# Performance work log

Measured on AMD Instinct MI355X. Metric: run time of the kernel, lower is better.

The kernel has to match this reference:

```python
import jax, jax.numpy as jnp
import numpy as np

D = 1024; HEADS = 16; DH = D // HEADS; DEPTH = 8; FACT = 2
EPS = 1e-6


def _rmsnorm(x):
    return x * jax.lax.rsqrt(jnp.mean(x * x, axis=-1, keepdims=True) + EPS)


def _rope(x, pos):
    # x: [N, H, T, d]; pos: [T]. Standard rotate-half RoPE on dim d.
    d = x.shape[-1]
    half = d // 2
    inv_freq = 1.0 / (10000.0 ** (jnp.arange(half, dtype=x.dtype) / half))
    ang = pos[:, None] * inv_freq  # [T, half]
    cos = jnp.concatenate([jnp.cos(ang), jnp.cos(ang)], axis=-1)  # [T, d]
    sin = jnp.concatenate([jnp.sin(ang), jnp.sin(ang)], axis=-1)
    rot = jnp.concatenate([-x[..., half:], x[..., :half]], axis=-1)
    return x * cos + rot * sin


def _apply_rope_2d(q, k, pos_h, pos_w):
    # Split head_dim in half: first half rotated by row position, second by column.
    dh = q.shape[-1] // 2
    q = jnp.concatenate([_rope(q[..., :dh], pos_h), _rope(q[..., dh:], pos_w)], axis=-1)
    k = jnp.concatenate([_rope(k[..., :dh], pos_h), _rope(k[..., dh:], pos_w)], axis=-1)
    return q, k


def setup_inputs() -> dict:
    key = jax.random.key(0)
    ks = jax.random.split(key, 8)
    s = 0.02
    f32 = jnp.float32
    return {
        "x": jax.random.normal(ks[0], (4, 16, 64, 64), f32),
        "merge_w": (jax.random.normal(ks[1], (D, 16 * FACT * FACT), f32) * s),
        "qkv_w": (jax.random.normal(ks[2], (DEPTH, 3 * D, D), f32) * s),
        "qkv_b": jnp.zeros((DEPTH, 3 * D), f32),
        "proj_w": (jax.random.normal(ks[3], (DEPTH, D, D), f32) * s),
        "proj_b": jnp.zeros((DEPTH, D), f32),
        "fc1_w": (jax.random.normal(ks[4], (DEPTH, 4 * D, D), f32) * s),
        "fc1_b": jnp.zeros((DEPTH, 4 * D), f32),
        "fc2_w": (jax.random.normal(ks[5], (DEPTH, D, 4 * D), f32) * s),
        "fc2_b": jnp.zeros((DEPTH, D), f32),
    }


def reference(x, merge_w, qkv_w, qkv_b, proj_w, proj_b, fc1_w, fc1_b, fc2_w, fc2_b):
    N, C, H, W = x.shape
    Hf, Wf = H // FACT, W // FACT
    L = Hf * Wf
    # SpatialMerger: unfold(k=f,s=f) channel order is (c, kh, kw)
    patches = x.reshape(N, C, Hf, FACT, Wf, FACT)
    patches = patches.transpose(0, 2, 4, 1, 3, 5).reshape(N, L, C * FACT * FACT)
    tok = patches @ merge_w.T  # [N, L, D], bias=False

    pos_h = jnp.repeat(jnp.arange(Hf, dtype=tok.dtype), Wf)  # [L]
    pos_w = jnp.tile(jnp.arange(Wf, dtype=tok.dtype), Hf)
    scale = 1.0 / np.sqrt(DH)

    for i in range(DEPTH):
        h = _rmsnorm(tok)
        qkv = h @ qkv_w[i].T + qkv_b[i]  # [N, L, 3D]
        q, k, v = jnp.split(qkv, 3, axis=-1)
        q = q.reshape(N, L, HEADS, DH).transpose(0, 2, 1, 3)  # [N, Hh, T, Dh]
        k = k.reshape(N, L, HEADS, DH).transpose(0, 2, 1, 3)
        v = v.reshape(N, L, HEADS, DH).transpose(0, 2, 1, 3)
        q, k = _apply_rope_2d(q, k, pos_h, pos_w)
        attn = jnp.einsum('nhtd,nhsd->nhts', q, k) * scale
        p = jax.nn.softmax(attn, axis=-1)
        o = jnp.einsum('nhts,nhsd->nhtd', p, v)
        o = o.transpose(0, 2, 1, 3).reshape(N, L, D)
        tok = tok + (o @ proj_w[i].T + proj_b[i])

        h = _rmsnorm(tok)
        hidden = jax.nn.gelu(h @ fc1_w[i].T + fc1_b[i], approximate=True)
        tok = tok + (hidden @ fc2_w[i].T + fc2_b[i])

    z_seq = _rmsnorm(tok)          # [N, L, D]
    z = z_seq.transpose(0, 2, 1)   # [N, D, L]
    return z
```

## Files before the change

kernel.cpp:

```cpp
#include <hip/hip_runtime.h>
#include <hip/hip_bf16.h>
#include <cmath>

typedef __bf16 bf16_t;
typedef __bf16 bf16x4 __attribute__((ext_vector_type(4)));
typedef __bf16 bf16x8 __attribute__((ext_vector_type(8)));
typedef float f32x4 __attribute__((ext_vector_type(4)));

typedef const __attribute__((address_space(1))) void gv_t;
typedef __attribute__((address_space(3))) void sv_t;

#define GLDS16(g, l) __builtin_amdgcn_global_load_lds((gv_t*)(g), (sv_t*)(l), 16, 0, 0)

template <int EPI>
__global__ __launch_bounds__(256, 2) void gemm128(
    const bf16_t* __restrict__ A, const bf16_t* __restrict__ B,
    const float* __restrict__ bias, float* __restrict__ Cf,
    bf16_t* __restrict__ Cb, int N, int K, int KS)
{
    __shared__ __align__(16) bf16_t As[3][128 * 32];
    __shared__ __align__(16) bf16_t Bs[3][128 * 32];
    const int tid = threadIdx.x;
    const int bm = blockIdx.x, bn = blockIdx.y, bz = blockIdx.z;
    const int wave = tid >> 6, lane = tid & 63;
    const int wr = (wave >> 1) << 6, wc = (wave & 1) << 6;
    const int lr = lane & 15, kq = (lane >> 4) << 3;

    f32x4 acc[4][4] = {};

    const int kbeg = bz * KS;
    const bf16_t* gA = A + (size_t)(bm * 128 + (tid >> 2)) * K + (tid & 3) * 8 + kbeg;
    const bf16_t* gB = B + (size_t)(bn * 128 + (tid >> 2)) * K + (tid & 3) * 8 + kbeg;
    const bf16_t* gA2 = gA + (size_t)64 * K;
    const bf16_t* gB2 = gB + (size_t)64 * K;
    const int dst = tid * 8;
    const int nt = KS >> 5;

#define STAGE(buf, t) do { const int _k = (t) << 5;          \
        GLDS16(gA  + _k, As[buf] + dst);                     \
        GLDS16(gA2 + _k, As[buf] + dst + 2048);              \
        GLDS16(gB  + _k, Bs[buf] + dst);                     \
        GLDS16(gB2 + _k, Bs[buf] + dst + 2048); } while (0)

    STAGE(0, 0);
    if (nt > 1) STAGE(1, 1);
    int cur = 0, pre = 2;
    for (int t = 0; t < nt; ++t) {
        if (t + 1 < nt) asm volatile("s_waitcnt vmcnt(4)" ::: "memory");
        else            asm volatile("s_waitcnt vmcnt(0)" ::: "memory");
        __builtin_amdgcn_s_barrier();
        if (t + 2 < nt) STAGE(pre, t + 2);

        const bf16_t* Ac = As[cur];
        const bf16_t* Bc = Bs[cur];
        bf16x8 af[4], bfr[4];
#pragma unroll
        for (int i = 0; i < 4; i++)
            af[i] = *(const bf16x8*)(Ac + (wr + i * 16 + lr) * 32 + kq);
#pragma unroll
        for (int j = 0; j < 4; j++)
            bfr[j] = *(const bf16x8*)(Bc + (wc + j * 16 + lr) * 32 + kq);
#pragma unroll
        for (int i = 0; i < 4; i++)
#pragma unroll
            for (int j = 0; j < 4; j++)
                acc[i][j] = __builtin_amdgcn_mfma_f32_16x16x32_bf16(af[i], bfr[j], acc[i][j], 0, 0, 0);

        cur = (cur == 2) ? 0 : cur + 1;
        pre = (pre == 2) ? 0 : pre + 1;
    }
#undef STAGE

    const int row0 = bm * 128 + wr + ((lane >> 4) << 2);
    const int col0 = bn * 128 + wc + lr;

    if constexpr (EPI == 6) {
        float bv[4];
#pragma unroll
        for (int j = 0; j < 4; j++) bv[j] = bias[col0 + j * 16];
        const bool doRope = (col0 < 2048);
        const float invf = exp2f(-0.83048202372184056f * (float)lr);
#pragma unroll
        for (int i = 0; i < 4; i++) {
#pragma unroll
            for (int r = 0; r < 4; r++) {
                const int row = row0 + i * 16 + r;
                float v0 = acc[i][0][r] + bv[0], v1 = acc[i][1][r] + bv[1];
                float v2 = acc[i][2][r] + bv[2], v3 = acc[i][3][r] + bv[3];
                if (doRope) {
                    const int tt = row & 1023;
                    float s0, c0, s1, c1;
                    sincosf((float)(tt >> 5) * invf, &s0, &c0);
                    sincosf((float)(tt & 31) * invf, &s1, &c1);
                    float o0 = v0 * c0 - v1 * s0, o1 = v1 * c0 + v0 * s0;
                    float o2 = v2 * c1 - v3 * s1, o3 = v3 * c1 + v2 * s1;
                    v0 = o0; v1 = o1; v2 = o2; v3 = o3;
                }
                bf16_t* cp = Cb + (size_t)row * N + col0;
                cp[0] = (bf16_t)v0; cp[16] = (bf16_t)v1;
                cp[32] = (bf16_t)v2; cp[48] = (bf16_t)v3;
            }
        }
        return;
    }

#pragma unroll
    for (int j = 0; j < 4; j++) {
        const int col = col0 + j * 16;
        float bv = 0.f;
        if constexpr (EPI == 5) { if (bz == 0) bv = bias[col]; }
        else if constexpr (EPI != 0) bv = bias[col];
#pragma unroll
        for (int i = 0; i < 4; i++) {
#pragma unroll
            for (int r = 0; r < 4; r++) {
                const int row = row0 + i * 16 + r;
                float v = acc[i][j][r] + bv;
                if constexpr (EPI == 0) {
                    Cf[(size_t)row * N + col] = v;
                } else if constexpr (EPI == 5) {
                    atomicAdd(&Cf[(size_t)row * 1024 + col], v);
                } else if constexpr (EPI == 3) {
                    float g = 0.5f * v * (1.f + tanhf(0.7978845608f * (v + 0.044715f * v * v * v)));
                    Cb[(size_t)row * N + col] = (bf16_t)g;
                } else {
                    Cb[(size_t)row * N + col] = (bf16_t)v;
                }
            }
        }
    }
}

__global__ __launch_bounds__(256) void convw_k(
    const float* __restrict__ q, const float* __restrict__ p,
    const float* __restrict__ f1, const float* __restrict__ f2,
    bf16_t* __restrict__ oq, bf16_t* __restrict__ op,
    bf16_t* __restrict__ of1, bf16_t* __restrict__ of2)
{
    int idx = blockIdx.x * 256 + threadIdx.x;
    const float* src; bf16_t* dst; int off;
    if (idx < 786432)       { src = q;  dst = oq;  off = idx; }
    else if (idx < 1048576) { src = p;  dst = op;  off = idx - 786432; }
    else if (idx < 2097152) { src = f1; dst = of1; off = idx - 1048576; }
    else                    { src = f2; dst = of2; off = idx - 2097152; }
    float4 v = ((const float4*)src)[off];
    bf16x4 o; o[0] = (bf16_t)v.x; o[1] = (bf16_t)v.y; o[2] = (bf16_t)v.z; o[3] = (bf16_t)v.w;
    *(bf16x4*)(dst + (size_t)off * 4) = o;
}

__global__ __launch_bounds__(256) void cvt_k(const float* __restrict__ in, bf16_t* __restrict__ out)
{
    int idx = blockIdx.x * 256 + threadIdx.x;
    float4 v = ((const float4*)in)[idx];
    bf16x4 o; o[0] = (bf16_t)v.x; o[1] = (bf16_t)v.y; o[2] = (bf16_t)v.z; o[3] = (bf16_t)v.w;
    *(bf16x4*)(out + (size_t)idx * 4) = o;
}

__global__ __launch_bounds__(256) void patches_k(const float* __restrict__ x, bf16_t* __restrict__ out)
{
    int idx = blockIdx.x * 256 + threadIdx.x;
    int cc = idx & 63, l = (idx >> 6) & 1023, n = idx >> 16;
    int c = cc >> 2, kh = (cc >> 1) & 1, kw = cc & 1;
    int hf = l >> 5, wf = l & 31;
    out[idx] = (bf16_t)x[(((n * 16 + c) * 64) + hf * 2 + kh) * 64 + wf * 2 + kw];
}

__global__ __launch_bounds__(256) void rmsnorm_k(const float* __restrict__ tok, bf16_t* __restrict__ out)
{
    int row = blockIdx.x, tid = threadIdx.x;
    float4 xv = ((const float4*)(tok + (size_t)row * 1024))[tid];
    float s = xv.x * xv.x + xv.y * xv.y + xv.z * xv.z + xv.w * xv.w;
#pragma unroll
    for (int off = 32; off > 0; off >>= 1) s += __shfl_down(s, off, 64);
    __shared__ float ws4[4];
    if ((tid & 63) == 0) ws4[tid >> 6] = s;
    __syncthreads();
    float sc = rsqrtf((ws4[0] + ws4[1] + ws4[2] + ws4[3]) * (1.f / 1024.f) + 1e-6f);
    bf16_t* o = out + (size_t)row * 1024 + tid * 4;
    bf16x4 ov;
    ov[0] = (bf16_t)(xv.x * sc); ov[1] = (bf16_t)(xv.y * sc);
    ov[2] = (bf16_t)(xv.z * sc); ov[3] = (bf16_t)(xv.w * sc);
    *(bf16x4*)o = ov;
}

__global__ __launch_bounds__(256) void vtrans_k(const bf16_t* __restrict__ qkv, bf16_t* __restrict__ vt)
{
    __shared__ bf16_t tile[64][72];
    const int tid = threadIdx.x, b = blockIdx.x;
    const int tt = b & 15, h = (b >> 4) & 15, n = b >> 8;
#pragma unroll
    for (int rr = 0; rr < 2; rr++) {
        int idx = rr * 256 + tid;
        int tr = idx >> 3, dc = (idx & 7) * 8;
        bf16x8 v = *(const bf16x8*)(qkv + (size_t)(n * 1024 + tt * 64 + tr) * 3072 + 2048 + h * 64 + dc);
        *(bf16x8*)&tile[tr][dc] = v;
    }
    __syncthreads();
#pragma unroll
    for (int rr = 0; rr < 2; rr++) {
        int idx = rr * 256 + tid;
        int d = idx >> 3, tc = (idx & 7) * 8;
        bf16x8 ov;
#pragma unroll
        for (int e = 0; e < 8; e++) ov[e] = tile[tc + e][d];
        *(bf16x8*)(vt + (size_t)((n * 16 + h) * 64 + d) * 1024 + tt * 64 + tc) = ov;
    }
}

__global__ __launch_bounds__(256, 2) void attn_mfma(
    const bf16_t* __restrict__ qkv, const bf16_t* __restrict__ vt, bf16_t* __restrict__ obuf)
{
    __shared__ __align__(16) bf16_t Ks[64 * 64];
    __shared__ __align__(16) bf16_t Vs[64 * 64];
    __shared__ __align__(16) bf16_t Ps[4][32 * 64];

    const int tid = threadIdx.x, wave = tid >> 6, lane = tid & 63;
    const int lr = lane & 15, g = lane >> 4;
    const int blk = blockIdx.x;
    const int qb = blk & 7, h = (blk >> 3) & 15, n = blk >> 7;
    const int t0 = qb * 128 + wave * 32;

    bf16x8 bq[2][2];
#pragma unroll
    for (int j = 0; j < 2; j++)
#pragma unroll
        for (int kk = 0; kk < 2; kk++) {
            bf16x8 v = *(const bf16x8*)(qkv + (size_t)(n * 1024 + t0 + j * 16 + lr) * 3072 + h * 64 + kk * 32 + g * 8);
#pragma unroll
            for (int e = 0; e < 8; e++) v[e] = (bf16_t)((float)v[e] * 0.125f);
            bq[j][kk] = v;
        }

    f32x4 o[2][4] = {};
    float m[2] = {-1e30f, -1e30f}, l[2] = {0.f, 0.f};

    const int sr = tid >> 3, pcb = tid & 7;
    const int scb = (pcb ^ (sr & 7)) * 8;
    const bf16_t* ksrc = qkv + (size_t)(n * 1024 + sr) * 3072 + 1024 + h * 64 + scb;
    const bf16_t* vsrc = vt + (size_t)((n * 16 + h) * 64 + sr) * 1024 + scb;
    bf16_t* kdst = Ks + tid * 8;
    bf16_t* vdst = Vs + tid * 8;

    for (int s0 = 0; s0 < 1024; s0 += 64) {
        __syncthreads();
        GLDS16(ksrc + (size_t)s0 * 3072, kdst);
        GLDS16(ksrc + (size_t)(s0 + 32) * 3072, kdst + 2048);
        GLDS16(vsrc + s0, vdst);
        GLDS16(vsrc + s0 + (size_t)32 * 1024, vdst + 2048);
        __syncthreads();

        f32x4 st[4][2] = {};
#pragma unroll
        for (int kk = 0; kk < 2; kk++) {
            bf16x8 ak[4];
#pragma unroll
            for (int i = 0; i < 4; i++)
                ak[i] = *(const bf16x8*)((const char*)Ks + (i * 16 + lr) * 128 + (((kk * 4 + g) ^ (lr & 7)) * 16));
#pragma unroll
            for (int i = 0; i < 4; i++)
#pragma unroll
                for (int j = 0; j < 2; j++)
                    st[i][j] = __builtin_amdgcn_mfma_f32_16x16x32_bf16(ak[i], bq[j][kk], st[i][j], 0, 0, 0);
        }

        float al2[2];
#pragma unroll
        for (int j = 0; j < 2; j++) {
            float rm = st[0][j][0];
#pragma unroll
            for (int i = 0; i < 4; i++)
#pragma unroll
                for (int r = 0; r < 4; r++) rm = fmaxf(rm, st[i][j][r]);
            rm = fmaxf(rm, __shfl_xor(rm, 16, 64));
            rm = fmaxf(rm, __shfl_xor(rm, 32, 64));
            float mn = fmaxf(m[j], rm);
            float al = __expf(m[j] - mn);
            m[j] = mn; al2[j] = al;
            float ps = 0.f;
#pragma unroll
            for (int i = 0; i < 4; i++) {
                bf16x4 pk;
#pragma unroll
                for (int r = 0; r < 4; r++) {
                    float p = __expf(st[i][j][r] - mn);
                    bf16_t pb = (bf16_t)p;
                    pk[r] = pb;
                    ps += (float)pb;
                }
                *(bf16x4*)((char*)&Ps[wave][0] + (j * 16 + lr) * 128 +
                           (((i * 2 + (g >> 1)) ^ (lr & 7)) * 16) + (g & 1) * 8) = pk;
            }
            ps += __shfl_xor(ps, 16, 64);
            ps += __shfl_xor(ps, 32, 64);
            l[j] = l[j] * al + ps;
        }

#pragma unroll
        for (int ti = 0; ti < 2; ti++)
#pragma unroll
            for (int r = 0; r < 4; r++) {
                float av = __shfl(al2[ti], g * 4 + r, 64);
#pragma unroll
                for (int dj = 0; dj < 4; dj++) o[ti][dj][r] *= av;
            }

#pragma unroll
        for (int kk = 0; kk < 2; kk++) {
            bf16x8 ap[2], bv[4];
#pragma unroll
            for (int ti = 0; ti < 2; ti++)
                ap[ti] = *(const bf16x8*)((const char*)&Ps[wave][0] + (ti * 16 + lr) * 128 +
                                          (((kk * 4 + g) ^ (lr & 7)) * 16));
#pragma unroll
            for (int dj = 0; dj < 4; dj++)
                bv[dj] = *(const bf16x8*)((const char*)Vs + (dj * 16 + lr) * 128 +
                                          (((kk * 4 + g) ^ (lr & 7)) * 16));
#pragma unroll
            for (int ti = 0; ti < 2; ti++)
#pragma unroll
                for (int dj = 0; dj < 4; dj++)
                    o[ti][dj] = __builtin_amdgcn_mfma_f32_16x16x32_bf16(ap[ti], bv[dj], o[ti][dj], 0, 0, 0);
        }
    }

#pragma unroll
    for (int ti = 0; ti < 2; ti++)
#pragma unroll
        for (int r = 0; r < 4; r++) {
            float lv = __shfl(l[ti], g * 4 + r, 64);
            float inv = 1.f / lv;
            const int trow = n * 1024 + qb * 128 + wave * 32 + ti * 16 + g * 4 + r;
#pragma unroll
            for (int dj = 0; dj < 4; dj++)
                obuf[(size_t)trow * 1024 + h * 64 + dj * 16 + lr] = (bf16_t)(o[ti][dj][r] * inv);
        }
}

__global__ __launch_bounds__(256) void rmsscale_k(const float* __restrict__ tok, float* __restrict__ scale)
{
    int row = blockIdx.x, tid = threadIdx.x;
    float4 xv = ((const float4*)(tok + (size_t)row * 1024))[tid];
    float s = xv.x * xv.x + xv.y * xv.y + xv.z * xv.z + xv.w * xv.w;
#pragma unroll
    for (int off = 32; off > 0; off >>= 1) s += __shfl_down(s, off, 64);
    __shared__ float ws4[4];
    if ((tid & 63) == 0) ws4[tid >> 6] = s;
    __syncthreads();
    if (tid == 0)
        scale[row] = rsqrtf((ws4[0] + ws4[1] + ws4[2] + ws4[3]) * (1.f / 1024.f) + 1e-6f);
}

__global__ __launch_bounds__(256) void transpose_out_k(const float* __restrict__ tok,
                                                       const float* __restrict__ scale,
                                                       float* __restrict__ out)
{
    __shared__ float tile[64][65];
    const int tid = threadIdx.x;
    const int tt = blockIdx.x * 64, dd = blockIdx.y * 64, n = blockIdx.z;
#pragma unroll
    for (int rb = 0; rb < 4; rb++) {
        int tl = rb * 16 + (tid >> 4);
        int cl = (tid & 15) * 4;
        float4 v = *(const float4*)(tok + (size_t)(n * 1024 + tt + tl) * 1024 + dd + cl);
        float sc = scale[n * 1024 + tt + tl];
        tile[cl + 0][tl] = v.x * sc;
        tile[cl + 1][tl] = v.y * sc;
        tile[cl + 2][tl] = v.z * sc;
        tile[cl + 3][tl] = v.w * sc;
    }
    __syncthreads();
#pragma unroll
    for (int rb = 0; rb < 4; rb++) {
        int dl = rb * 16 + (tid >> 4);
        int tl = (tid & 15) * 4;
        float4 v = make_float4(tile[dl][tl + 0], tile[dl][tl + 1], tile[dl][tl + 2], tile[dl][tl + 3]);
        *(float4*)(out + (size_t)n * 1024 * 1024 + (size_t)(dd + dl) * 1024 + tt + tl) = v;
    }
}

extern "C" void kernel_launch(void* const* d_in, const int* in_sizes, int n_in,
                              void* d_out, int out_size, void* d_ws, size_t ws_size,
                              hipStream_t stream)
{
    const float* x       = (const float*)d_in[0];
    const float* merge_w = (const float*)d_in[1];
    const float* qkv_w   = (const float*)d_in[2];
    const float* qkv_b   = (const float*)d_in[3];
    const float* proj_w  = (const float*)d_in[4];
    const float* proj_b  = (const float*)d_in[5];
    const float* fc1_w   = (const float*)d_in[6];
    const float* fc1_b   = (const float*)d_in[7];
    const float* fc2_w   = (const float*)d_in[8];
    const float* fc2_b   = (const float*)d_in[9];
    float* out = (float*)d_out;

    char* ws = (char*)d_ws;
    float*  tok   = (float*)ws;
    bf16_t* Ab    = (bf16_t*)(ws + (16u << 20));
    bf16_t* ob    = (bf16_t*)(ws + (24u << 20));
    bf16_t* qkvb  = (bf16_t*)(ws + (32u << 20));
    bf16_t* vtb   = (bf16_t*)(ws + (56u << 20));
    bf16_t* hid   = (bf16_t*)(ws + (32u << 20));
    bf16_t* wqkv  = (bf16_t*)(ws + (64u << 20));
    bf16_t* wproj = wqkv + (size_t)3072 * 1024;
    bf16_t* wfc1  = wproj + (size_t)1024 * 1024;
    bf16_t* wfc2  = wfc1 + (size_t)4096 * 1024;
    bf16_t* wmrg  = (bf16_t*)(ws + (90u << 20));
    float*  scl   = (float*)(ws + (91u << 20));

    cvt_k<<<64, 256, 0, stream>>>(merge_w, wmrg);
    patches_k<<<1024, 256, 0, stream>>>(x, Ab);
    gemm128<0><<<dim3(32, 8, 1), 256, 0, stream>>>(Ab, wmrg, nullptr, tok, nullptr, 1024, 64, 64);

    for (int i = 0; i < 8; i++) {
        convw_k<<<12288, 256, 0, stream>>>(
            qkv_w + (size_t)i * 3072 * 1024, proj_w + (size_t)i * 1024 * 1024,
            fc1_w + (size_t)i * 4096 * 1024, fc2_w + (size_t)i * 1024 * 4096,
            wqkv, wproj, wfc1, wfc2);

        rmsnorm_k<<<4096, 256, 0, stream>>>(tok, Ab);
        gemm128<6><<<dim3(32, 24, 1), 256, 0, stream>>>(Ab, wqkv, qkv_b + (size_t)i * 3072,
                                                        nullptr, qkvb, 3072, 1024, 1024);
        vtrans_k<<<1024, 256, 0, stream>>>(qkvb, vtb);
        attn_mfma<<<512, 256, 0, stream>>>(qkvb, vtb, ob);
        gemm128<5><<<dim3(32, 8, 2), 256, 0, stream>>>(ob, wproj, proj_b + (size_t)i * 1024,
                                                       tok, nullptr, 1024, 1024, 512);
        rmsnorm_k<<<4096, 256, 0, stream>>>(tok, Ab);
        gemm128<3><<<dim3(32, 32, 1), 256, 0, stream>>>(Ab, wfc1, fc1_b + (size_t)i * 4096,
                                                        nullptr, hid, 4096, 1024, 1024);
        gemm128<5><<<dim3(32, 8, 2), 256, 0, stream>>>(hid, wfc2, fc2_b + (size_t)i * 1024,
                                                       tok, nullptr, 1024, 4096, 2048);
    }
    rmsscale_k<<<4096, 256, 0, stream>>>(tok, scl);
    transpose_out_k<<<dim3(16, 16, 4), 256, 0, stream>>>(tok, scl, out);
}
```

Measured before the change: 2.514 ms.

## Replace split-K atomic adds with partial buffer merged in next rmsnorm

The split-K residual GEMMs (proj and fc2) no longer use float atomicAdd into the residual stream. The first K-slice does a plain read-modify-write into tok and the second writes its partial to a separate buffer. The following rmsnorm (or the final rms-scale) adds that partial back into tok before normalizing. Workspace buffers are reassigned so the partials can alias freed regions, which trades atomic traffic for an extra buffer write and read.

```diff
diff --git a/kernel.cpp b/kernel.cpp
--- a/kernel.cpp
+++ b/kernel.cpp
@@ -16,7 +16,7 @@
 __global__ __launch_bounds__(256, 2) void gemm128(
     const bf16_t* __restrict__ A, const bf16_t* __restrict__ B,
     const float* __restrict__ bias, float* __restrict__ Cf,
-    bf16_t* __restrict__ Cb, int N, int K, int KS)
+    float* __restrict__ Cf2, bf16_t* __restrict__ Cb, int N, int K, int KS)
 {
     __shared__ __align__(16) bf16_t As[3][128 * 32];
     __shared__ __align__(16) bf16_t Bs[3][128 * 32];
@@ -108,8 +108,8 @@
     for (int j = 0; j < 4; j++) {
         const int col = col0 + j * 16;
         float bv = 0.f;
+        if constexpr (EPI == 3) bv = bias[col];
         if constexpr (EPI == 5) { if (bz == 0) bv = bias[col]; }
-        else if constexpr (EPI != 0) bv = bias[col];
 #pragma unroll
         for (int i = 0; i < 4; i++) {
 #pragma unroll
@@ -119,12 +119,15 @@
                 if constexpr (EPI == 0) {
                     Cf[(size_t)row * N + col] = v;
                 } else if constexpr (EPI == 5) {
-                    atomicAdd(&Cf[(size_t)row * 1024 + col], v);
+                    if (bz == 0) {
+                        float* dp = Cf + (size_t)row * 1024 + col;
+                        *dp += v;
+                    } else {
+                        Cf2[(size_t)row * 1024 + col] = v;
+                    }
                 } else if constexpr (EPI == 3) {
                     float g = 0.5f * v * (1.f + tanhf(0.7978845608f * (v + 0.044715f * v * v * v)));
                     Cb[(size_t)row * N + col] = (bf16_t)g;
-                } else {
-                    Cb[(size_t)row * N + col] = (bf16_t)v;
                 }
             }
         }
@@ -165,10 +168,17 @@
     out[idx] = (bf16_t)x[(((n * 16 + c) * 64) + hf * 2 + kh) * 64 + wf * 2 + kw];
 }
 
-__global__ __launch_bounds__(256) void rmsnorm_k(const float* __restrict__ tok, bf16_t* __restrict__ out)
+__global__ __launch_bounds__(256) void rmsnorm_k(float* __restrict__ tok,
+                                                 const float* __restrict__ p,
+                                                 bf16_t* __restrict__ out)
 {
     int row = blockIdx.x, tid = threadIdx.x;
     float4 xv = ((const float4*)(tok + (size_t)row * 1024))[tid];
+    if (p) {
+        float4 pv = ((const float4*)(p + (size_t)row * 1024))[tid];
+        xv.x += pv.x; xv.y += pv.y; xv.z += pv.z; xv.w += pv.w;
+        ((float4*)(tok + (size_t)row * 1024))[tid] = xv;
+    }
     float s = xv.x * xv.x + xv.y * xv.y + xv.z * xv.z + xv.w * xv.w;
 #pragma unroll
     for (int off = 32; off > 0; off >>= 1) s += __shfl_down(s, off, 64);
@@ -336,10 +346,17 @@
         }
 }
 
-__global__ __launch_bounds__(256) void rmsscale_k(const float* __restrict__ tok, float* __restrict__ scale)
+__global__ __launch_bounds__(256) void rmsscale_k(float* __restrict__ tok,
+                                                  const float* __restrict__ p,
+                                                  float* __restrict__ scale)
 {
     int row = blockIdx.x, tid = threadIdx.x;
     float4 xv = ((const float4*)(tok + (size_t)row * 1024))[tid];
+    if (p) {
+        float4 pv = ((const float4*)(p + (size_t)row * 1024))[tid];
+        xv.x += pv.x; xv.y += pv.y; xv.z += pv.z; xv.w += pv.w;
+        ((float4*)(tok + (size_t)row * 1024))[tid] = xv;
+    }
     float s = xv.x * xv.x + xv.y * xv.y + xv.z * xv.z + xv.w * xv.w;
 #pragma unroll
     for (int off = 32; off > 0; off >>= 1) s += __shfl_down(s, off, 64);
@@ -396,10 +413,13 @@
 
     char* ws = (char*)d_ws;
     float*  tok   = (float*)ws;
-    bf16_t* Ab    = (bf16_t*)(ws + (16u << 20));
+    float*  pfc2  = (float*)(ws + (16u << 20));
+    bf16_t* vtb   = (bf16_t*)(ws + (16u << 20));
+    bf16_t* A2    = (bf16_t*)(ws + (16u << 20));
     bf16_t* ob    = (bf16_t*)(ws + (24u << 20));
-    bf16_t* qkvb  = (bf16_t*)(ws + (32u << 20));
-    bf16_t* vtb   = (bf16_t*)(ws + (56u << 20));
+    bf16_t* A1    = (bf16_t*)(ws + (32u << 20));
+    bf16_t* qkvb  = (bf16_t*)(ws + (40u << 20));
+    float*  pproj = (float*)(ws + (40u << 20));
     bf16_t* hid   = (bf16_t*)(ws + (32u << 20));
     bf16_t* wqkv  = (bf16_t*)(ws + (64u << 20));
     bf16_t* wproj = wqkv + (size_t)3072 * 1024;
@@ -409,8 +429,8 @@
     float*  scl   = (float*)(ws + (91u << 20));
 
     cvt_k<<<64, 256, 0, stream>>>(merge_w, wmrg);
-    patches_k<<<1024, 256, 0, stream>>>(x, Ab);
-    gemm128<0><<<dim3(32, 8, 1), 256, 0, stream>>>(Ab, wmrg, nullptr, tok, nullptr, 1024, 64, 64);
+    patches_k<<<1024, 256, 0, stream>>>(x, A1);
+    gemm128<0><<<dim3(32, 8, 1), 256, 0, stream>>>(A1, wmrg, nullptr, tok, nullptr, nullptr, 1024, 64, 64);
 
     for (int i = 0; i < 8; i++) {
         convw_k<<<12288, 256, 0, stream>>>(
@@ -418,19 +438,19 @@
             fc1_w + (size_t)i * 4096 * 1024, fc2_w + (size_t)i * 1024 * 4096,
             wqkv, wproj, wfc1, wfc2);
 
-        rmsnorm_k<<<4096, 256, 0, stream>>>(tok, Ab);
-        gemm128<6><<<dim3(32, 24, 1), 256, 0, stream>>>(Ab, wqkv, qkv_b + (size_t)i * 3072,
-                                                        nullptr, qkvb, 3072, 1024, 1024);
+        rmsnorm_k<<<4096, 256, 0, stream>>>(tok, i == 0 ? nullptr : pfc2, A1);
+        gemm128<6><<<dim3(32, 24, 1), 256, 0, stream>>>(A1, wqkv, qkv_b + (size_t)i * 3072,
+                                                        nullptr, nullptr, qkvb, 3072, 1024, 1024);
         vtrans_k<<<1024, 256, 0, stream>>>(qkvb, vtb);
         attn_mfma<<<512, 256, 0, stream>>>(qkvb, vtb, ob);
         gemm128<5><<<dim3(32, 8, 2), 256, 0, stream>>>(ob, wproj, proj_b + (size_t)i * 1024,
-                                                       tok, nullptr, 1024, 1024, 512);
-        rmsnorm_k<<<4096, 256, 0, stream>>>(tok, Ab);
-        gemm128<3><<<dim3(32, 32, 1), 256, 0, stream>>>(Ab, wfc1, fc1_b + (size_t)i * 4096,
-                                                        nullptr, hid, 4096, 1024, 1024);
+                                                       tok, pproj, nullptr, 1024, 1024, 512);
+        rmsnorm_k<<<4096, 256, 0, stream>>>(tok, pproj, A2);
+        gemm128<3><<<dim3(32, 32, 1), 256, 0, stream>>>(A2, wfc1, fc1_b + (size_t)i * 4096,
+                                                        nullptr, nullptr, hid, 4096, 1024, 1024);
         gemm128<5><<<dim3(32, 8, 2), 256, 0, stream>>>(hid, wfc2, fc2_b + (size_t)i * 1024,
-                                                       tok, nullptr, 1024, 4096, 2048);
-    }
-    rmsscale_k<<<4096, 256, 0, stream>>>(tok, scl);
+                                                       tok, pfc2, nullptr, 1024, 4096, 2048);
+    }
+    rmsscale_k<<<4096, 256, 0, stream>>>(tok, pfc2, scl);
     transpose_out_k<<<dim3(16, 16, 4), 256, 0, stream>>>(tok, scl, out);
 }
```

Result: no change. 2.470 ms (-1.7%).
